# Performance work log

Hardware: AMD Instinct MI355X
Metric: run time of the kernel (lower is better)

## Reference

```python
import jax, jax.numpy as jnp
import numpy as np


def setup_inputs() -> dict:
    key = jax.random.key(0)
    # Uniform in (0.9, 1.1) so the running product over 8192 elements stays finite.
    x = jax.random.uniform(key, (4096, 8192), dtype=jnp.float32, minval=0.9, maxval=1.1)
    return {"x": x}


def reference(x) -> jnp.ndarray:
    # Inclusive prefix product along dim 1 (matches cumprod_dim1_cuda / torch.cumprod(x, dim=1)).
    return jnp.cumprod(x, axis=1)
```

## Files before the change

### kernel.cpp

```cpp
#include <hip/hip_runtime.h>


#define N     8192
#define T     256
#define WPB   (T / 64)
#define TILE  1024
#define NT    (N / TILE)
#define CHK   (TILE / 256)

typedef float f32x4 __attribute__((ext_vector_type(4)));
typedef const __attribute__((address_space(1))) float glb_f;
typedef __attribute__((address_space(3))) float lds_f;

__device__ __forceinline__ float readlane63(float x) {
    return __builtin_bit_cast(float,
        __builtin_amdgcn_readlane(__builtin_bit_cast(int, x), 63));
}

template<int CTRL, int RM, int BM>
__device__ __forceinline__ float dpp_id1(float x) {
    int r = __builtin_amdgcn_update_dpp(
        __builtin_bit_cast(int, 1.0f), __builtin_bit_cast(int, x),
        CTRL, RM, BM, false);
    return __builtin_bit_cast(float, r);
}

__device__ __forceinline__ float wave_scan_mul(float x) {
    x *= dpp_id1<0x111, 0xf, 0xf>(x);
    x *= dpp_id1<0x112, 0xf, 0xf>(x);
    x *= dpp_id1<0x114, 0xf, 0xf>(x);
    x *= dpp_id1<0x118, 0xf, 0xf>(x);
    x *= dpp_id1<0x142, 0xa, 0xf>(x);
    x *= dpp_id1<0x143, 0xc, 0xf>(x);
    return x;
}

__global__ __launch_bounds__(T) void cumprod_rows_kernel(
    const float* __restrict__ x, float* __restrict__ out, int n_rows)
{
    __shared__ float lds[WPB][2][TILE];

    const int lane = threadIdx.x & 63;
    const int wid  = threadIdx.x >> 6;
    const int row  = blockIdx.x * WPB + wid;
    if (row >= n_rows) return;

    const float* __restrict__ xr   = x   + (size_t)row * N;
    float*       __restrict__ outr = out + (size_t)row * N;

#pragma unroll
    for (int c = 0; c < CHK; ++c)
        __builtin_amdgcn_global_load_lds(
            (glb_f*)(xr + c * 256 + lane * 4),
            (lds_f*)&lds[wid][0][c * 256], 16, 0, 0);

    float carry = 1.0f;

#pragma unroll
    for (int t = 0; t < NT; ++t) {
        const int b = t & 1;

        if (t + 1 < NT) {
#pragma unroll
            for (int c = 0; c < CHK; ++c)
                __builtin_amdgcn_global_load_lds(
                    (glb_f*)(xr + (t + 1) * TILE + c * 256 + lane * 4),
                    (lds_f*)&lds[wid][b ^ 1][c * 256], 16, 0, 0);
        }

        if (t == 0 || t == NT - 1)
            asm volatile("s_waitcnt vmcnt(4)" ::: "memory");
        else
            asm volatile("s_waitcnt vmcnt(8)" ::: "memory");
        __builtin_amdgcn_sched_barrier(0);

        f32x4 d[CHK];
        float coef[CHK];
#pragma unroll
        for (int c = 0; c < CHK; ++c) {
            d[c] = *reinterpret_cast<const f32x4*>(
                       &lds[wid][b][c * 256 + lane * 4]);
            d[c].y *= d[c].x;
            d[c].z *= d[c].y;
            d[c].w *= d[c].z;
            const float tt = d[c].w;
            const float e  = __shfl_up(tt, 1, 64);
            const float ep = (lane == 0) ? 1.0f : e;
            const float exc = wave_scan_mul(ep);
            coef[c] = carry * exc;
            carry  *= readlane63(exc * tt);
        }

#pragma unroll
        for (int c = 0; c < CHK; ++c) {
            f32x4 o = d[c];
            o.x *= coef[c]; o.y *= coef[c];
            o.z *= coef[c]; o.w *= coef[c];
            __builtin_nontemporal_store(
                o, reinterpret_cast<f32x4*>(outr + t * TILE + c * 256 + lane * 4));
        }
    }
}

extern "C" void kernel_launch(void* const* d_in, const int* in_sizes, int n_in,
                              void* d_out, int out_size, void* d_ws, size_t ws_size,
                              hipStream_t stream)
{
    const float* x   = (const float*)d_in[0];
    float*       out = (float*)d_out;
    const int n_rows = in_sizes[0] / N;
    const int nblk   = (n_rows + WPB - 1) / WPB;
    cumprod_rows_kernel<<<nblk, T, 0, stream>>>(x, out, n_rows);
}
```

Before: 228.5 us.

## Deepen per-wave LDS prefetch pipeline to four smaller tiles

Replaces the double-buffered 1024-element tiles with a four-deep ring of 512-element tiles per wave. Three tiles are kept in flight ahead of compute, and vmcnt waits are derived from outstanding loads and stores. A refill is issued into the just-consumed slot only after the scan has read it. This keeps more memory requests in flight to hide HBM latency, at the cost of more complex wait accounting and a dependence on the compiler's exact instruction ordering.

```diff
diff --git a/kernel.cpp b/kernel.cpp
--- a/kernel.cpp
+++ b/kernel.cpp
@@ -1,12 +1,13 @@
 #include <hip/hip_runtime.h>
 
 
-#define N     8192
-#define T     256
-#define WPB   (T / 64)
-#define TILE  1024
-#define NT    (N / TILE)
-#define CHK   (TILE / 256)
+#define N      8192
+#define T      256
+#define WPB    (T / 64)
+#define TILE   512
+#define NT     (N / TILE)
+#define CHK    (TILE / 256)
+#define DEPTH  4
 
 typedef float f32x4 __attribute__((ext_vector_type(4)));
 typedef const __attribute__((address_space(1))) float glb_f;
@@ -35,10 +36,21 @@
     return x;
 }
 
+__device__ __forceinline__ void wait_vm(int vm) {
+    if      (vm >= 14) asm volatile("s_waitcnt vmcnt(14)" ::: "memory");
+    else if (vm == 12) asm volatile("s_waitcnt vmcnt(12)" ::: "memory");
+    else if (vm == 10) asm volatile("s_waitcnt vmcnt(10)" ::: "memory");
+    else if (vm == 8)  asm volatile("s_waitcnt vmcnt(8)"  ::: "memory");
+    else if (vm == 6)  asm volatile("s_waitcnt vmcnt(6)"  ::: "memory");
+    else if (vm == 4)  asm volatile("s_waitcnt vmcnt(4)"  ::: "memory");
+    else if (vm == 2)  asm volatile("s_waitcnt vmcnt(2)"  ::: "memory");
+    else               asm volatile("s_waitcnt vmcnt(0)"  ::: "memory");
+}
+
 __global__ __launch_bounds__(T) void cumprod_rows_kernel(
     const float* __restrict__ x, float* __restrict__ out, int n_rows)
 {
-    __shared__ float lds[WPB][2][TILE];
+    __shared__ float lds[WPB][DEPTH][TILE];
 
     const int lane = threadIdx.x & 63;
     const int wid  = threadIdx.x >> 6;
@@ -49,29 +61,24 @@
     float*       __restrict__ outr = out + (size_t)row * N;
 
 #pragma unroll
-    for (int c = 0; c < CHK; ++c)
-        __builtin_amdgcn_global_load_lds(
-            (glb_f*)(xr + c * 256 + lane * 4),
-            (lds_f*)&lds[wid][0][c * 256], 16, 0, 0);
+    for (int t = 0; t < DEPTH; ++t)
+#pragma unroll
+        for (int c = 0; c < CHK; ++c)
+            __builtin_amdgcn_global_load_lds(
+                (glb_f*)(xr + t * TILE + c * 256 + lane * 4),
+                (lds_f*)&lds[wid][t][c * 256], 16, 0, 0);
 
     float carry = 1.0f;
 
 #pragma unroll
     for (int t = 0; t < NT; ++t) {
-        const int b = t & 1;
+        const int b = t % DEPTH;
 
-        if (t + 1 < NT) {
-#pragma unroll
-            for (int c = 0; c < CHK; ++c)
-                __builtin_amdgcn_global_load_lds(
-                    (glb_f*)(xr + (t + 1) * TILE + c * 256 + lane * 4),
-                    (lds_f*)&lds[wid][b ^ 1][c * 256], 16, 0, 0);
+        {
+            const int nl = (NT - 1 - t < DEPTH - 1) ? (NT - 1 - t) : (DEPTH - 1);
+            const int ns = (t < DEPTH) ? t : DEPTH;
+            wait_vm(2 * (nl + ns));
         }
-
-        if (t == 0 || t == NT - 1)
-            asm volatile("s_waitcnt vmcnt(4)" ::: "memory");
-        else
-            asm volatile("s_waitcnt vmcnt(8)" ::: "memory");
         __builtin_amdgcn_sched_barrier(0);
 
         f32x4 d[CHK];
@@ -89,6 +96,15 @@
             const float exc = wave_scan_mul(ep);
             coef[c] = carry * exc;
             carry  *= readlane63(exc * tt);
+        }
+        __builtin_amdgcn_sched_barrier(0);
+
+        if (t + DEPTH < NT) {
+#pragma unroll
+            for (int c = 0; c < CHK; ++c)
+                __builtin_amdgcn_global_load_lds(
+                    (glb_f*)(xr + (t + DEPTH) * TILE + c * 256 + lane * 4),
+                    (lds_f*)&lds[wid][b][c * 256], 16, 0, 0);
         }
 
 #pragma unroll
```

New measurement: 230.6 us. About the same (+0.9%).
